# Kernel tuning notes

Measured on AMD Instinct MI355X. Metric: run time of the kernel, lower is better.

The kernel has to match this reference:

```python
import jax, jax.numpy as jnp
import numpy as np


def _unfold(x, r):
    # x: [b, ch, h, w] -> [b, ch, k*k, h, w], zero-padded 3x3-style neighborhoods
    b, ch, h, w = x.shape
    k = 2 * r + 1
    xp = jnp.pad(x, ((0, 0), (0, 0), (r, r), (r, r)))
    patches = [xp[:, :, i:i + h, j:j + w] for i in range(k) for j in range(k)]
    return jnp.stack(patches, axis=2)


def setup_inputs() -> dict:
    key = jax.random.key(0)
    ks = jax.random.split(key, 6)
    b, c, h, w = 4, 128, 128, 128
    scale = 1.0 / np.sqrt(c)
    return {
        "feature0": jax.random.normal(ks[0], (b, c, h, w), jnp.float32),
        "flow": jax.random.normal(ks[1], (b, 2, h, w), jnp.float32),
        "q_w": jax.random.normal(ks[2], (c, c), jnp.float32) * scale,
        "q_b": jax.random.normal(ks[3], (c,), jnp.float32) * 0.01,
        "k_w": jax.random.normal(ks[4], (c, c), jnp.float32) * scale,
        "k_b": jax.random.normal(ks[5], (c,), jnp.float32) * 0.01,
        "local_window_attn": 1,
        "local_window_radius": 1,
    }


def reference(feature0, flow, q_w, q_b, k_w, k_b, local_window_attn, local_window_radius):
    b, c, h, w = feature0.shape
    inv_sqrt_c = 1.0 / jnp.sqrt(jnp.asarray(c, feature0.dtype))
    x = feature0.reshape(b, c, h * w).transpose(0, 2, 1)  # [b, hw, c]
    q = x @ q_w.T + q_b  # q_proj
    if local_window_attn:
        r = local_window_radius
        kf = x @ k_w.T + k_b  # k_proj applied to original feature
        kmap = kf.transpose(0, 2, 1).reshape(b, c, h, w)
        kwin = _unfold(kmap, r)      # [b, c, k2, h, w]
        fwin = _unfold(flow, r)      # [b, 2, k2, h, w]
        qmap = q.reshape(b, h, w, c)
        scores = jnp.einsum('bhwc,bckhw->bhwk', qmap, kwin) * inv_sqrt_c
        prob = jax.nn.softmax(scores, axis=-1)
        out = jnp.einsum('bhwk,bfkhw->bfhw', prob, fwin)  # [b, 2, h, w]
        return out
    else:
        # NOTE: faithful to source, key = k_proj(q_proj(x))
        key_ = q @ k_w.T + k_b
        value = flow.reshape(b, flow.shape[1], h * w).transpose(0, 2, 1)  # [b, hw, 2]
        scores = jnp.einsum('bnc,bmc->bnm', q, key_) * inv_sqrt_c
        prob = jax.nn.softmax(scores, axis=-1)
        out = jnp.einsum('bnm,bmf->bnf', prob, value)
        return out.reshape(b, h, w, value.shape[-1]).transpose(0, 3, 1, 2)
```

## Files before the change

kernel.cpp:

```cpp
#include <hip/hip_runtime.h>


#define HW 16384
#define NB 4
#define TOT (NB * HW)

typedef short bf16x8 __attribute__((ext_vector_type(8)));
typedef float f32x4 __attribute__((ext_vector_type(4)));

__device__ __forceinline__ unsigned short f2bf(float f) {
    unsigned u = __float_as_uint(f);
    return (unsigned short)((u + 0x7fffu + ((u >> 16) & 1u)) >> 16);
}
__device__ __forceinline__ float bf2f(unsigned short s) {
    return __uint_as_float(((unsigned)s) << 16);
}

__global__ void prep_kernel(const float* __restrict__ qw, const float* __restrict__ qb,
                            const float* __restrict__ kw, const float* __restrict__ kb,
                            unsigned short* __restrict__ Mh, unsigned short* __restrict__ Ml,
                            float* __restrict__ u, float* __restrict__ v,
                            float* __restrict__ dptr) {
    __shared__ float red[128];
    int bid = blockIdx.x, tid = threadIdx.x;
    if (bid < 16) {
        int ci = bid * 8 + (tid >> 5);
        int cj = (tid & 31) * 4;
        float4 acc = make_float4(0.f, 0.f, 0.f, 0.f);
#pragma unroll 4
        for (int co = 0; co < 128; ++co) {
            float qv = qw[co * 128 + ci];
            float4 kv = *(const float4*)(kw + co * 128 + cj);
            acc.x += qv * kv.x; acc.y += qv * kv.y;
            acc.z += qv * kv.z; acc.w += qv * kv.w;
        }
        int o = ci * 128 + cj;
        float a[4] = {acc.x, acc.y, acc.z, acc.w};
#pragma unroll
        for (int j = 0; j < 4; ++j) {
            unsigned short h = f2bf(a[j]);
            Mh[o + j] = h;
            Ml[o + j] = f2bf(a[j] - bf2f(h));
        }
    } else {
        int half = tid >> 7, t = tid & 127;
        const float* w  = half ? kw : qw;
        const float* bv = half ? qb : kb;
        float acc = 0.f;
#pragma unroll 4
        for (int co = 0; co < 128; ++co) acc += w[co * 128 + t] * bv[co];
        if (half) v[t] = acc; else u[t] = acc;
        if (!half) red[t] = qb[t] * kb[t];
        __syncthreads();
        if (tid == 0) {
            float dd = 0.f;
            for (int i = 0; i < 128; ++i) dd += red[i];
            *dptr = dd;
        }
    }
}

__global__ __launch_bounds__(256, 2)
void proj_kernel(const float* __restrict__ feat, const unsigned short* __restrict__ MhG,
                 const unsigned short* __restrict__ MlG, float* __restrict__ y) {
    int tid = threadIdx.x;
    int W = blockIdx.x * 4 + (tid >> 6);
    int lane = tid & 63;
    int cig = W & 3, pxg = W >> 2;
    int ci0 = cig * 32;
    int P0 = pxg * 64;
    int b = P0 >> 14, p0 = P0 & (HW - 1);
    int m = lane & 15, q = lane >> 4;
    const float* xbase = feat + (size_t)b * 128 * HW + p0;

    f32x4 zero = {0.f, 0.f, 0.f, 0.f};
    f32x4 acc[2][4];
#pragma unroll
    for (int t = 0; t < 2; ++t)
#pragma unroll
        for (int s = 0; s < 4; ++s) acc[t][s] = zero;

#pragma unroll
    for (int kc = 0; kc < 4; ++kc) {
        int c0 = kc * 32;
        bf16x8 ah[2], al[2];
#pragma unroll
        for (int t = 0; t < 2; ++t) {
            int roff = (ci0 + t * 16 + m) * 128 + c0 + q * 8;
            ah[t] = *(const bf16x8*)(MhG + roff);
            al[t] = *(const bf16x8*)(MlG + roff);
        }
        bf16x8 bh[4], bl[4];
#pragma unroll
        for (int s = 0; s < 4; ++s) {
            const float* xp = xbase + (size_t)(c0 + q * 8) * HW + s * 16 + m;
            float xv[8];
#pragma unroll
            for (int j = 0; j < 8; ++j) xv[j] = xp[(size_t)j * HW];
#pragma unroll
            for (int j = 0; j < 8; ++j) {
                unsigned short h = f2bf(xv[j]);
                bh[s][j] = (short)h;
                bl[s][j] = (short)f2bf(xv[j] - bf2f(h));
            }
        }
#pragma unroll
        for (int t = 0; t < 2; ++t)
#pragma unroll
            for (int s = 0; s < 4; ++s) {
                acc[t][s] = __builtin_amdgcn_mfma_f32_16x16x32_bf16(ah[t], bh[s], acc[t][s], 0, 0, 0);
                acc[t][s] = __builtin_amdgcn_mfma_f32_16x16x32_bf16(ah[t], bl[s], acc[t][s], 0, 0, 0);
                acc[t][s] = __builtin_amdgcn_mfma_f32_16x16x32_bf16(al[t], bh[s], acc[t][s], 0, 0, 0);
            }
    }

    int rg = lane >> 4, col = lane & 15;
#pragma unroll
    for (int t = 0; t < 2; ++t)
#pragma unroll
        for (int s = 0; s < 4; ++s) {
            float* yp = y + ((size_t)b * 128 + ci0 + t * 16 + rg * 4) * HW + p0 + s * 16 + col;
#pragma unroll
            for (int r = 0; r < 4; ++r) yp[(size_t)r * HW] = acc[t][s][r];
        }
}

__global__ __launch_bounds__(256, 4)
void attn_partial_kernel(const float* __restrict__ feat, const float* __restrict__ y,
                         const float* __restrict__ u, const float* __restrict__ v,
                         float* __restrict__ ps, float* __restrict__ gd) {
    int tid = threadIdx.x;
    int blk = blockIdx.x;
    int cg = blk >> 7;
    int pp = (blk & 127) * 256 + tid;
    int P = pp * 2;
    int b = P >> 14;
    int p = P & (HW - 1);
    const float* xb = feat + ((size_t)b * 128 + cg * 32) * HW + p;
    const float* yb = y + ((size_t)b * 128 + cg * 32) * HW + p;

    float s0[9], s1[9];
#pragma unroll
    for (int k = 0; k < 9; ++k) { s0[k] = 0.f; s1[k] = 0.f; }
    float g0 = 0.f, g1 = 0.f, d0 = 0.f, d1 = 0.f;

#pragma unroll 2
    for (int c = 0; c < 32; ++c) {
        float2 xv = *(const float2*)(xb + (size_t)c * HW);
        float uc = u[cg * 32 + c], vc = v[cg * 32 + c];
        g0 += xv.x * uc; g1 += xv.y * uc;
        d0 += xv.x * vc; d1 += xv.y * vc;
        const float* yc = yb + (size_t)c * HW;
#pragma unroll
        for (int dy = 0; dy < 3; ++dy) {
            const float* yr = yc + (dy - 1) * 128;
            float2 a  = *(const float2*)(yr - 2);
            float2 bb = *(const float2*)(yr);
            float2 cc = *(const float2*)(yr + 2);
            s0[dy * 3 + 0] += xv.x * a.y;   s1[dy * 3 + 0] += xv.y * bb.x;
            s0[dy * 3 + 1] += xv.x * bb.x;  s1[dy * 3 + 1] += xv.y * bb.y;
            s0[dy * 3 + 2] += xv.x * bb.y;  s1[dy * 3 + 2] += xv.y * cc.x;
        }
    }
    float* pso = ps + (size_t)cg * 9 * TOT + P;
#pragma unroll
    for (int k = 0; k < 9; ++k)
        *(float2*)(pso + (size_t)k * TOT) = make_float2(s0[k], s1[k]);
    *(float2*)(gd + (size_t)(cg * 2 + 0) * TOT + P) = make_float2(g0, g1);
    *(float2*)(gd + (size_t)(cg * 2 + 1) * TOT + P) = make_float2(d0, d1);
}

__global__ __launch_bounds__(256, 4)
void attn_final_kernel(const float* __restrict__ flow, const float* __restrict__ ps,
                       const float* __restrict__ gd, const float* __restrict__ dptr,
                       float* __restrict__ out) {
    int P = blockIdx.x * 256 + threadIdx.x;
    int b = P >> 14, p = P & (HW - 1);
    int row = p >> 7, col = p & 127;
    const float inv = 0.08838834764831845f;
    float dconst = *dptr;

    float g = 0.f;
#pragma unroll
    for (int cg = 0; cg < 4; ++cg) g += gd[(size_t)(cg * 2) * TOT + P];

    float sc[9];
    float mx = -1e30f;
#pragma unroll
    for (int k = 0; k < 9; ++k) {
        int dy = k / 3 - 1, dx = (k % 3) - 1;
        bool valid = ((unsigned)(row + dy) < 128u) && ((unsigned)(col + dx) < 128u);
        float ssum = 0.f;
#pragma unroll
        for (int cg = 0; cg < 4; ++cg) ssum += ps[(size_t)(cg * 9 + k) * TOT + P];
        int Pn = P + dy * 128 + dx;
        Pn = max(0, min(TOT - 1, Pn));
        float dsum = dconst;
#pragma unroll
        for (int cg = 0; cg < 4; ++cg) dsum += gd[(size_t)(cg * 2 + 1) * TOT + Pn];
        float s = valid ? (ssum + g + dsum) * inv : 0.f;
        sc[k] = s;
        mx = fmaxf(mx, s);
    }
    float e[9], sum = 0.f;
#pragma unroll
    for (int k = 0; k < 9; ++k) { e[k] = __expf(sc[k] - mx); sum += e[k]; }
    float rs = 1.f / sum;

    float o0 = 0.f, o1 = 0.f;
#pragma unroll
    for (int k = 0; k < 9; ++k) {
        int dy = k / 3 - 1, dx = (k % 3) - 1;
        bool valid = ((unsigned)(row + dy) < 128u) && ((unsigned)(col + dx) < 128u);
        float pr = valid ? e[k] * rs : 0.f;
        int fi0 = b * 2 * HW + p + dy * 128 + dx;
        fi0 = max(0, min(2 * TOT - 1, fi0));
        int fi1 = (b * 2 + 1) * HW + p + dy * 128 + dx;
        fi1 = max(0, min(2 * TOT - 1, fi1));
        o0 += pr * flow[fi0];
        o1 += pr * flow[fi1];
    }
    out[(size_t)(b * 2) * HW + p] = o0;
    out[(size_t)(b * 2 + 1) * HW + p] = o1;
}

extern "C" void kernel_launch(void* const* d_in, const int* in_sizes, int n_in,
                              void* d_out, int out_size, void* d_ws, size_t ws_size,
                              hipStream_t stream) {
    const float* feat = (const float*)d_in[0];
    const float* flow = (const float*)d_in[1];
    const float* qw = (const float*)d_in[2];
    const float* qb = (const float*)d_in[3];
    const float* kw = (const float*)d_in[4];
    const float* kb = (const float*)d_in[5];

    float* ws = (float*)d_ws;
    float* u = ws;
    float* v = ws + 128;
    float* dptr = ws + 256;
    unsigned short* Mh = (unsigned short*)(ws + 512);
    unsigned short* Ml = (unsigned short*)(ws + 8704);
    float* y = ws + 16896;
    float* ps = ws + 8405760;
    float* gd = ws + 10765056;
    float* out = (float*)d_out;

    prep_kernel<<<17, 256, 0, stream>>>(qw, qb, kw, kb, Mh, Ml, u, v, dptr);
    proj_kernel<<<1024, 256, 0, stream>>>(feat, Mh, Ml, y);
    attn_partial_kernel<<<512, 256, 0, stream>>>(feat, y, u, v, ps, gd);
    attn_final_kernel<<<256, 256, 0, stream>>>(flow, ps, gd, dptr, out);
}
```

Before: 127.7 us.

## Fuse attention partial and final kernels via LDS, move g/d dots into projection

The partial-score and softmax kernels are merged into one 512-thread block. Per-channel-group partial scores are reduced through shared memory instead of a global scratch buffer, which removes the ps and gd round trips and one launch. The u·x and v·x dot products are now computed inside the projection kernel by the ci-group-0 waves, which write compact gmap/dmap arrays. The prep kernel is also spread over 128 blocks, each splitting the co reduction in two halves. The trade-offs are extra work in one quarter of the projection waves, fewer blocks for the fused attention kernel, and only half its threads active during the softmax phase.

```diff
diff --git a/kernel.cpp b/kernel.cpp
--- a/kernel.cpp
+++ b/kernel.cpp
@@ -23,24 +23,22 @@
                             float* __restrict__ dptr) {
     __shared__ float red[128];
     int bid = blockIdx.x, tid = threadIdx.x;
-    if (bid < 16) {
-        int ci = bid * 8 + (tid >> 5);
-        int cj = (tid & 31) * 4;
-        float4 acc = make_float4(0.f, 0.f, 0.f, 0.f);
+    if (bid < 128) {
+        int ci = bid;
+        int cj = tid & 127, half = tid >> 7;
+        int co0 = half * 64;
+        const float* qcol = qw + ci;
+        float acc = 0.f;
 #pragma unroll 4
-        for (int co = 0; co < 128; ++co) {
-            float qv = qw[co * 128 + ci];
-            float4 kv = *(const float4*)(kw + co * 128 + cj);
-            acc.x += qv * kv.x; acc.y += qv * kv.y;
-            acc.z += qv * kv.z; acc.w += qv * kv.w;
-        }
-        int o = ci * 128 + cj;
-        float a[4] = {acc.x, acc.y, acc.z, acc.w};
-#pragma unroll
-        for (int j = 0; j < 4; ++j) {
-            unsigned short h = f2bf(a[j]);
-            Mh[o + j] = h;
-            Ml[o + j] = f2bf(a[j] - bf2f(h));
+        for (int co = 0; co < 64; ++co)
+            acc += qcol[(size_t)(co0 + co) * 128] * kw[(size_t)(co0 + co) * 128 + cj];
+        if (half) red[cj] = acc;
+        __syncthreads();
+        if (!half) {
+            float mval = acc + red[cj];
+            unsigned short h = f2bf(mval);
+            Mh[ci * 128 + cj] = h;
+            Ml[ci * 128 + cj] = f2bf(mval - bf2f(h));
         }
     } else {
         int half = tid >> 7, t = tid & 127;
@@ -62,7 +60,9 @@
 
 __global__ __launch_bounds__(256, 2)
 void proj_kernel(const float* __restrict__ feat, const unsigned short* __restrict__ MhG,
-                 const unsigned short* __restrict__ MlG, float* __restrict__ y) {
+                 const unsigned short* __restrict__ MlG,
+                 const float* __restrict__ u, const float* __restrict__ v,
+                 float* __restrict__ y, float* __restrict__ gmap, float* __restrict__ dmap) {
     int tid = threadIdx.x;
     int W = blockIdx.x * 4 + (tid >> 6);
     int lane = tid & 63;
@@ -80,6 +80,9 @@
 #pragma unroll
         for (int s = 0; s < 4; ++s) acc[t][s] = zero;
 
+    float gacc[4] = {0.f, 0.f, 0.f, 0.f};
+    float dacc[4] = {0.f, 0.f, 0.f, 0.f};
+
 #pragma unroll
     for (int kc = 0; kc < 4; ++kc) {
         int c0 = kc * 32;
@@ -90,6 +93,14 @@
             ah[t] = *(const bf16x8*)(MhG + roff);
             al[t] = *(const bf16x8*)(MlG + roff);
         }
+        float uu[8], vv[8];
+        if (cig == 0) {
+#pragma unroll
+            for (int j = 0; j < 8; ++j) {
+                uu[j] = u[c0 + q * 8 + j];
+                vv[j] = v[c0 + q * 8 + j];
+            }
+        }
         bf16x8 bh[4], bl[4];
 #pragma unroll
         for (int s = 0; s < 4; ++s) {
@@ -97,6 +108,13 @@
             float xv[8];
 #pragma unroll
             for (int j = 0; j < 8; ++j) xv[j] = xp[(size_t)j * HW];
+            if (cig == 0) {
+#pragma unroll
+                for (int j = 0; j < 8; ++j) {
+                    gacc[s] += uu[j] * xv[j];
+                    dacc[s] += vv[j] * xv[j];
+                }
+            }
 #pragma unroll
             for (int j = 0; j < 8; ++j) {
                 unsigned short h = f2bf(xv[j]);
@@ -123,17 +141,34 @@
 #pragma unroll
             for (int r = 0; r < 4; ++r) yp[(size_t)r * HW] = acc[t][s][r];
         }
-}
-
-__global__ __launch_bounds__(256, 4)
-void attn_partial_kernel(const float* __restrict__ feat, const float* __restrict__ y,
-                         const float* __restrict__ u, const float* __restrict__ v,
-                         float* __restrict__ ps, float* __restrict__ gd) {
+
+    if (cig == 0) {
+#pragma unroll
+        for (int s = 0; s < 4; ++s) {
+            float gg = gacc[s];
+            gg += __shfl_xor(gg, 16);
+            gg += __shfl_xor(gg, 32);
+            float dd = dacc[s];
+            dd += __shfl_xor(dd, 16);
+            dd += __shfl_xor(dd, 32);
+            if (lane < 16) {
+                gmap[P0 + s * 16 + lane] = gg;
+                dmap[P0 + s * 16 + lane] = dd;
+            }
+        }
+    }
+}
+
+__global__ __launch_bounds__(512, 2)
+void attn_fused_kernel(const float* __restrict__ feat, const float* __restrict__ y,
+                       const float* __restrict__ gmap, const float* __restrict__ dmap,
+                       const float* __restrict__ dptr, const float* __restrict__ flow,
+                       float* __restrict__ out) {
+    __shared__ float2 lds[4 * 9 * 128];
     int tid = threadIdx.x;
-    int blk = blockIdx.x;
-    int cg = blk >> 7;
-    int pp = (blk & 127) * 256 + tid;
-    int P = pp * 2;
+    int cg = tid >> 7;
+    int pp = tid & 127;
+    int P = blockIdx.x * 256 + pp * 2;
     int b = P >> 14;
     int p = P & (HW - 1);
     const float* xb = feat + ((size_t)b * 128 + cg * 32) * HW + p;
@@ -142,14 +177,10 @@
     float s0[9], s1[9];
 #pragma unroll
     for (int k = 0; k < 9; ++k) { s0[k] = 0.f; s1[k] = 0.f; }
-    float g0 = 0.f, g1 = 0.f, d0 = 0.f, d1 = 0.f;
 
 #pragma unroll 2
     for (int c = 0; c < 32; ++c) {
         float2 xv = *(const float2*)(xb + (size_t)c * HW);
-        float uc = u[cg * 32 + c], vc = v[cg * 32 + c];
-        g0 += xv.x * uc; g1 += xv.y * uc;
-        d0 += xv.x * vc; d1 += xv.y * vc;
         const float* yc = yb + (size_t)c * HW;
 #pragma unroll
         for (int dy = 0; dy < 3; ++dy) {
@@ -162,66 +193,55 @@
             s0[dy * 3 + 2] += xv.x * bb.y;  s1[dy * 3 + 2] += xv.y * cc.x;
         }
     }
-    float* pso = ps + (size_t)cg * 9 * TOT + P;
 #pragma unroll
     for (int k = 0; k < 9; ++k)
-        *(float2*)(pso + (size_t)k * TOT) = make_float2(s0[k], s1[k]);
-    *(float2*)(gd + (size_t)(cg * 2 + 0) * TOT + P) = make_float2(g0, g1);
-    *(float2*)(gd + (size_t)(cg * 2 + 1) * TOT + P) = make_float2(d0, d1);
-}
-
-__global__ __launch_bounds__(256, 4)
-void attn_final_kernel(const float* __restrict__ flow, const float* __restrict__ ps,
-                       const float* __restrict__ gd, const float* __restrict__ dptr,
-                       float* __restrict__ out) {
-    int P = blockIdx.x * 256 + threadIdx.x;
-    int b = P >> 14, p = P & (HW - 1);
-    int row = p >> 7, col = p & 127;
-    const float inv = 0.08838834764831845f;
-    float dconst = *dptr;
-
-    float g = 0.f;
-#pragma unroll
-    for (int cg = 0; cg < 4; ++cg) g += gd[(size_t)(cg * 2) * TOT + P];
-
-    float sc[9];
-    float mx = -1e30f;
-#pragma unroll
-    for (int k = 0; k < 9; ++k) {
-        int dy = k / 3 - 1, dx = (k % 3) - 1;
-        bool valid = ((unsigned)(row + dy) < 128u) && ((unsigned)(col + dx) < 128u);
-        float ssum = 0.f;
-#pragma unroll
-        for (int cg = 0; cg < 4; ++cg) ssum += ps[(size_t)(cg * 9 + k) * TOT + P];
-        int Pn = P + dy * 128 + dx;
-        Pn = max(0, min(TOT - 1, Pn));
-        float dsum = dconst;
-#pragma unroll
-        for (int cg = 0; cg < 4; ++cg) dsum += gd[(size_t)(cg * 2 + 1) * TOT + Pn];
-        float s = valid ? (ssum + g + dsum) * inv : 0.f;
-        sc[k] = s;
-        mx = fmaxf(mx, s);
-    }
-    float e[9], sum = 0.f;
-#pragma unroll
-    for (int k = 0; k < 9; ++k) { e[k] = __expf(sc[k] - mx); sum += e[k]; }
-    float rs = 1.f / sum;
-
-    float o0 = 0.f, o1 = 0.f;
-#pragma unroll
-    for (int k = 0; k < 9; ++k) {
-        int dy = k / 3 - 1, dx = (k % 3) - 1;
-        bool valid = ((unsigned)(row + dy) < 128u) && ((unsigned)(col + dx) < 128u);
-        float pr = valid ? e[k] * rs : 0.f;
-        int fi0 = b * 2 * HW + p + dy * 128 + dx;
-        fi0 = max(0, min(2 * TOT - 1, fi0));
-        int fi1 = (b * 2 + 1) * HW + p + dy * 128 + dx;
-        fi1 = max(0, min(2 * TOT - 1, fi1));
-        o0 += pr * flow[fi0];
-        o1 += pr * flow[fi1];
-    }
-    out[(size_t)(b * 2) * HW + p] = o0;
-    out[(size_t)(b * 2 + 1) * HW + p] = o1;
+        lds[(cg * 9 + k) * 128 + pp] = make_float2(s0[k], s1[k]);
+    __syncthreads();
+
+    if (tid < 256) {
+        int P2 = blockIdx.x * 256 + tid;
+        int b2 = P2 >> 14, p2 = P2 & (HW - 1);
+        int row = p2 >> 7, col = p2 & 127;
+        const float inv = 0.08838834764831845f;
+        float dconst = *dptr;
+        float g = gmap[P2];
+        const float* lf = (const float*)lds;
+
+        float sc[9];
+        float mx = -1e30f;
+#pragma unroll
+        for (int k = 0; k < 9; ++k) {
+            float ssum = lf[(0 * 9 + k) * 256 + tid] + lf[(1 * 9 + k) * 256 + tid]
+                       + lf[(2 * 9 + k) * 256 + tid] + lf[(3 * 9 + k) * 256 + tid];
+            int dy = k / 3 - 1, dx = (k % 3) - 1;
+            bool valid = ((unsigned)(row + dy) < 128u) && ((unsigned)(col + dx) < 128u);
+            int Pn = P2 + dy * 128 + dx;
+            Pn = max(0, min(TOT - 1, Pn));
+            float s = valid ? (ssum + g + dconst + dmap[Pn]) * inv : 0.f;
+            sc[k] = s;
+            mx = fmaxf(mx, s);
+        }
+        float e[9], sum = 0.f;
+#pragma unroll
+        for (int k = 0; k < 9; ++k) { e[k] = __expf(sc[k] - mx); sum += e[k]; }
+        float rs = 1.f / sum;
+
+        float o0 = 0.f, o1 = 0.f;
+#pragma unroll
+        for (int k = 0; k < 9; ++k) {
+            int dy = k / 3 - 1, dx = (k % 3) - 1;
+            bool valid = ((unsigned)(row + dy) < 128u) && ((unsigned)(col + dx) < 128u);
+            float pr = valid ? e[k] * rs : 0.f;
+            int fi0 = b2 * 2 * HW + p2 + dy * 128 + dx;
+            fi0 = max(0, min(2 * TOT - 1, fi0));
+            int fi1 = (b2 * 2 + 1) * HW + p2 + dy * 128 + dx;
+            fi1 = max(0, min(2 * TOT - 1, fi1));
+            o0 += pr * flow[fi0];
+            o1 += pr * flow[fi1];
+        }
+        out[(size_t)(b2 * 2) * HW + p2] = o0;
+        out[(size_t)(b2 * 2 + 1) * HW + p2] = o1;
+    }
 }
 
 extern "C" void kernel_launch(void* const* d_in, const int* in_sizes, int n_in,
@@ -241,12 +261,11 @@
     unsigned short* Mh = (unsigned short*)(ws + 512);
     unsigned short* Ml = (unsigned short*)(ws + 8704);
     float* y = ws + 16896;
-    float* ps = ws + 8405760;
-    float* gd = ws + 10765056;
+    float* dmap = ws + 8405760;
+    float* gmap = ws + 8471296;
     float* out = (float*)d_out;
 
-    prep_kernel<<<17, 256, 0, stream>>>(qw, qb, kw, kb, Mh, Ml, u, v, dptr);
-    proj_kernel<<<1024, 256, 0, stream>>>(feat, Mh, Ml, y);
-    attn_partial_kernel<<<512, 256, 0, stream>>>(feat, y, u, v, ps, gd);
-    attn_final_kernel<<<256, 256, 0, stream>>>(flow, ps, gd, dptr, out);
-}
+    prep_kernel<<<129, 256, 0, stream>>>(qw, qb, kw, kb, Mh, Ml, u, v, dptr);
+    proj_kernel<<<1024, 256, 0, stream>>>(feat, Mh, Ml, u, v, y, gmap, dmap);
+    attn_fused_kernel<<<256, 512, 0, stream>>>(feat, y, gmap, dmap, dptr, flow, out);
+}
```

New measurement: 130.6 us. 1.02x slower.
